# Kernel optimization log

Measured on AMD Instinct MI355X. Metric: run time of the kernel, lower is better.

Reference implementation:

```python
import jax, jax.numpy as jnp
import numpy as np

N_NODES = 100000
N_EDGES = 1600000
IN_CH = 128
OUT_CH = 64


def setup_inputs() -> dict:
    key = jax.random.key(0)
    k1, k2, k3, k4, k5 = jax.random.split(key, 5)
    x = jax.random.normal(k1, (N_NODES, IN_CH), dtype=jnp.float32)
    edge_index = jax.random.randint(k2, (2, N_EDGES), 0, N_NODES, dtype=jnp.int64)
    edge_weight = jax.random.uniform(k3, (N_EDGES,), dtype=jnp.float32)
    # GCNConv linear weight (glorot-ish scale) and bias
    W = jax.random.normal(k4, (IN_CH, OUT_CH), dtype=jnp.float32) / np.float32(np.sqrt(IN_CH))
    b = jax.random.normal(k5, (OUT_CH,), dtype=jnp.float32) * 0.01
    return {"x": x, "edge_index": edge_index, "edge_weight": edge_weight, "W": W, "b": b}


def reference(x, edge_index, edge_weight, W, b):
    # PyG GCNConv with add_self_loops=False, normalize=True, followed by Sigmoid.
    row = edge_index[0]  # source nodes [E]
    col = edge_index[1]  # target nodes [E]
    n = x.shape[0]

    # gcn_norm (no self loops): deg[j] = sum of edge_weight into j
    deg = jax.ops.segment_sum(edge_weight, col, num_segments=n)  # [N]
    deg_inv_sqrt = jnp.where(deg > 0, jax.lax.rsqrt(deg), jnp.float32(0))
    norm = deg_inv_sqrt[row] * edge_weight * deg_inv_sqrt[col]  # [E]

    # linear transform then gather-scale-scatter aggregation
    h = x @ W  # [N, OUT]
    msg = norm[:, None] * h[row]  # [E, OUT]
    out = jax.ops.segment_sum(msg, col, num_segments=n) + b  # [N, OUT]
    return jax.nn.sigmoid(out)
```

## Files before the change

### kernel.cpp

```cpp
#include <hip/hip_runtime.h>

#define IN_CH 128
#define OUT_CH 64
#define BN 64
#define CAP 1280
#define NPART 256

typedef __attribute__((ext_vector_type(8))) short short8;
typedef __attribute__((ext_vector_type(4))) float f32x4;

__device__ __forceinline__ unsigned short f2bf(float f) {
    unsigned u = __float_as_uint(f);
    unsigned r = (u + 0x7FFFu + ((u >> 16) & 1u)) >> 16;
    return (unsigned short)r;
}

__global__ __launch_bounds__(1024) void k_part2(const int* __restrict__ row,
                                                const int* __restrict__ col,
                                                const float* __restrict__ ew,
                                                int* __restrict__ cnt,
                                                uint2* __restrict__ sparse,
                                                int E, int per, int nbuck) {
    __shared__ uint2 srec[6272];
    __shared__ unsigned short sbin[6272];
    __shared__ int loff[1600];
    __shared__ int lcur[1600];
    __shared__ int gbase[1600];
    __shared__ int wpart[16];
    __shared__ int stot;

    int tid = threadIdx.x;
    int e0 = blockIdx.x * per;
    int e1 = min(E, e0 + per);
    int nloc = e1 - e0;

    for (int i = tid; i < nbuck; i += 1024) loff[i] = 0;
    __syncthreads();

    for (int e = e0 + tid; e < e1; e += 1024)
        atomicAdd(&loff[col[e] >> 6], 1);
    __syncthreads();

    int b0 = 2 * tid, b1 = 2 * tid + 1;
    int s0 = (b0 < nbuck) ? loff[b0] : 0;
    int s1 = (b1 < nbuck) ? loff[b1] : 0;
    int ts = s0 + s1;
    int lane = tid & 63, wv = tid >> 6;
    int v = ts;
#pragma unroll
    for (int d = 1; d < 64; d <<= 1) { int t = __shfl_up(v, d, 64); if (lane >= d) v += t; }
    if (lane == 63) wpart[wv] = v;
    __syncthreads();
    if (tid < 16) {
        int vv = wpart[tid];
#pragma unroll
        for (int d = 1; d < 16; d <<= 1) { int t = __shfl_up(vv, d, 16); if (tid >= d) vv += t; }
        wpart[tid] = vv;
        if (tid == 15) stot = vv;
    }
    __syncthreads();
    int excl = ((wv > 0) ? wpart[wv - 1] : 0) + (v - ts);
    if (b0 < nbuck) loff[b0] = excl;
    if (b1 < nbuck) loff[b1] = excl + s0;
    __syncthreads();

    int total = stot;
    for (int b = tid; b < nbuck; b += 1024) {
        int nxt = (b + 1 < nbuck) ? loff[b + 1] : total;
        int c = nxt - loff[b];
        gbase[b] = c ? atomicAdd(&cnt[b], c) : 0;
        lcur[b] = loff[b];
    }
    __syncthreads();

    for (int e = e0 + tid; e < e1; e += 1024) {
        int r = row[e];
        int c = col[e];
        float w = ew[e];
        int bin = c >> 6;
        int p = atomicAdd(&lcur[bin], 1);
        srec[p] = make_uint2((unsigned)r | ((unsigned)(c & 63) << 17),
                             __float_as_uint(w));
        sbin[p] = (unsigned short)bin;
    }
    __syncthreads();

    for (int i = tid; i < nloc; i += 1024) {
        int bin = sbin[i];
        int k = i - loff[bin];
        int gp = gbase[bin] + k;
        if (gp < CAP)
            sparse[(size_t)bin * CAP + gp] = srec[i];
    }
}

__global__ __launch_bounds__(256) void k_gemm3(const float* __restrict__ x,
                                               const float* __restrict__ W,
                                               const uint2* __restrict__ sparse,
                                               const int* __restrict__ cnt,
                                               float* __restrict__ dis,
                                               unsigned short* __restrict__ hb,
                                               int N) {
    __shared__ unsigned short Wl[64][136];
    __shared__ float degs[BN];

    int tid = threadIdx.x;
    int b = blockIdx.x;
    int row0 = b * BN;

    if (tid < BN) degs[tid] = 0.f;
    __syncthreads();

    for (int i = tid; i < 2048; i += 256) {
        int k = i >> 4;
        int n4 = (i & 15) << 2;
        float4 v = *(const float4*)(W + (size_t)k * OUT_CH + n4);
        Wl[n4 + 0][k] = f2bf(v.x);
        Wl[n4 + 1][k] = f2bf(v.y);
        Wl[n4 + 2][k] = f2bf(v.z);
        Wl[n4 + 3][k] = f2bf(v.w);
    }
    {
        int m = min(cnt[b], CAP);
        int sbase = b * CAP;
        for (int i = tid; i < m; i += 256) {
            uint2 r = sparse[sbase + i];
            atomicAdd(&degs[(r.x >> 17) & 63], __uint_as_float(r.y));
        }
    }
    __syncthreads();

    if (tid < BN) {
        float d = degs[tid];
        float dv = (d > 0.f) ? rsqrtf(d) : 0.f;
        int node = row0 + tid;
        if (node < N) dis[node] = dv;
        degs[tid] = dv;
    }

    int lane = tid & 63;
    int wv = tid >> 6;
    int r0l = 16 * wv;
    int cn = lane & 15;
    int rg = lane >> 4;

    f32x4 acc0 = {0.f, 0.f, 0.f, 0.f};
    f32x4 acc1 = {0.f, 0.f, 0.f, 0.f};
    f32x4 acc2 = {0.f, 0.f, 0.f, 0.f};
    f32x4 acc3 = {0.f, 0.f, 0.f, 0.f};

    int arow = row0 + r0l + cn;
#pragma unroll
    for (int ks = 0; ks < 4; ++ks) {
        int k0 = ks * 32 + rg * 8;
        short8 a = {};
        if (arow < N) {
            const float* xp = x + (size_t)arow * IN_CH + k0;
            float4 va = *(const float4*)(xp);
            float4 vb = *(const float4*)(xp + 4);
            a[0] = (short)f2bf(va.x); a[1] = (short)f2bf(va.y);
            a[2] = (short)f2bf(va.z); a[3] = (short)f2bf(va.w);
            a[4] = (short)f2bf(vb.x); a[5] = (short)f2bf(vb.y);
            a[6] = (short)f2bf(vb.z); a[7] = (short)f2bf(vb.w);
        }
        short8 b0 = *(const short8*)&Wl[ 0 + cn][k0];
        short8 b1 = *(const short8*)&Wl[16 + cn][k0];
        short8 b2 = *(const short8*)&Wl[32 + cn][k0];
        short8 b3 = *(const short8*)&Wl[48 + cn][k0];
        acc0 = __builtin_amdgcn_mfma_f32_16x16x32_bf16(a, b0, acc0, 0, 0, 0);
        acc1 = __builtin_amdgcn_mfma_f32_16x16x32_bf16(a, b1, acc1, 0, 0, 0);
        acc2 = __builtin_amdgcn_mfma_f32_16x16x32_bf16(a, b2, acc2, 0, 0, 0);
        acc3 = __builtin_amdgcn_mfma_f32_16x16x32_bf16(a, b3, acc3, 0, 0, 0);
    }
    __syncthreads();

#pragma unroll
    for (int r = 0; r < 4; ++r) {
        int row_l = r0l + rg * 4 + r;
        int grow = row0 + row_l;
        if (grow < N) {
            float sc = degs[row_l];
            unsigned short* hp = hb + (size_t)grow * OUT_CH + cn;
            hp[ 0] = f2bf(acc0[r] * sc);
            hp[16] = f2bf(acc1[r] * sc);
            hp[32] = f2bf(acc2[r] * sc);
            hp[48] = f2bf(acc3[r] * sc);
        }
    }
}

__global__ __launch_bounds__(256) void k_sort3(const uint2* __restrict__ sparse,
                                               const int* __restrict__ cnt,
                                               const float* __restrict__ dis,
                                               const unsigned short* __restrict__ hb,
                                               const float* __restrict__ bias,
                                               float* __restrict__ out,
                                               int N, int nbuck) {
    __shared__ uint2 recbuf[CAP];
    __shared__ uint2 recbuf2[CAP];
    __shared__ int hist[BN];
    __shared__ int cur[BN];
    __shared__ int starts[BN];

    int b = blockIdx.x;
    int tid = threadIdx.x;
    int sbase = b * CAP;
    int m = min(cnt[b], CAP);

    if (tid < BN) hist[tid] = 0;
    __syncthreads();

    for (int i = tid; i < m; i += 256) {
        uint2 r = sparse[sbase + i];
        recbuf[i] = r;
        atomicAdd(&hist[(r.x >> 17) & 63], 1);
    }
    __syncthreads();

    if (tid < 64) {
        int h = hist[tid];
        int v = h;
#pragma unroll
        for (int d = 1; d < 64; d <<= 1) {
            int t = __shfl_up(v, d, 64);
            if (tid >= d) v += t;
        }
        int excl = v - h;
        cur[tid] = excl;
        starts[tid] = excl;
    }
    __syncthreads();

    for (int i = tid; i < m; i += 256) {
        uint2 r = recbuf[i];
        int dl = (r.x >> 17) & 63;
        int p = atomicAdd(&cur[dl], 1);
        recbuf2[p] = make_uint2(r.x & 0x1FFFF, r.y);
    }
    __syncthreads();

    int hwl = tid >> 5;
    int lanep = tid & 31;
    unsigned co = 2u * (unsigned)lanep;
    for (int nl = hwl; nl < BN; nl += 8) {
        int node = b * BN + nl;
        if (node >= N) break;
        int e = starts[nl];
        int e1 = e + hist[nl];
        float accx = 0.f, accy = 0.f;
        for (; e + 3 < e1; e += 4) {
            uint2 p0 = recbuf2[e];
            uint2 p1 = recbuf2[e + 1];
            uint2 p2 = recbuf2[e + 2];
            uint2 p3 = recbuf2[e + 3];
            unsigned v0 = *(const unsigned*)(hb + (p0.x << 6) + co);
            unsigned v1 = *(const unsigned*)(hb + (p1.x << 6) + co);
            unsigned v2 = *(const unsigned*)(hb + (p2.x << 6) + co);
            unsigned v3 = *(const unsigned*)(hb + (p3.x << 6) + co);
            float w0 = __uint_as_float(p0.y), w1 = __uint_as_float(p1.y);
            float w2 = __uint_as_float(p2.y), w3 = __uint_as_float(p3.y);
            accx += w0 * __uint_as_float(v0 << 16);
            accy += w0 * __uint_as_float(v0 & 0xFFFF0000u);
            accx += w1 * __uint_as_float(v1 << 16);
            accy += w1 * __uint_as_float(v1 & 0xFFFF0000u);
            accx += w2 * __uint_as_float(v2 << 16);
            accy += w2 * __uint_as_float(v2 & 0xFFFF0000u);
            accx += w3 * __uint_as_float(v3 << 16);
            accy += w3 * __uint_as_float(v3 & 0xFFFF0000u);
        }
        for (; e < e1; ++e) {
            uint2 p = recbuf2[e];
            unsigned v = *(const unsigned*)(hb + (p.x << 6) + co);
            float w = __uint_as_float(p.y);
            accx += w * __uint_as_float(v << 16);
            accy += w * __uint_as_float(v & 0xFFFF0000u);
        }
        float dd = dis[node];
        float2 bb = *(const float2*)(bias + co);
        float2 o;
        o.x = 1.f / (1.f + __expf(-(accx * dd + bb.x)));
        o.y = 1.f / (1.f + __expf(-(accy * dd + bb.y)));
        *(float2*)(out + ((size_t)node << 6) + co) = o;
    }
}

extern "C" void kernel_launch(void* const* d_in, const int* in_sizes, int n_in,
                              void* d_out, int out_size, void* d_ws, size_t ws_size,
                              hipStream_t stream) {
    const float* x   = (const float*)d_in[0];
    const int*   ei  = (const int*)d_in[1];
    const float* ew  = (const float*)d_in[2];
    const float* W   = (const float*)d_in[3];
    const float* b   = (const float*)d_in[4];
    float* out = (float*)d_out;

    const int N = in_sizes[0] / IN_CH;
    const int E = in_sizes[1] / 2;
    const int* row = ei;
    const int* col = ei + E;

    const int nbuck = (N + BN - 1) / BN;
    const int per   = (E + NPART - 1) / NPART;

    char* p = (char*)d_ws;
    int*   cnt     = (int*)p;    p += (size_t)nbuck * 4;
    float* dis     = (float*)p;  p += (size_t)N * 4;
    uint2* sparse  = (uint2*)p;  p += (size_t)nbuck * CAP * 8;
    unsigned short* hb = (unsigned short*)p;

    hipMemsetAsync(cnt, 0, (size_t)nbuck * 4, stream);

    k_part2<<<NPART, 1024, 0, stream>>>(row, col, ew, cnt, sparse, E, per, nbuck);
    k_gemm3<<<nbuck, 256, 0, stream>>>(x, W, sparse, cnt, dis, hb, N);
    k_sort3<<<nbuck, 256, 0, stream>>>(sparse, cnt, dis, hb, b, out, N, nbuck);
}
```

Before: 192.1 us.

## Fuse partition, GEMM and aggregation into one cooperative persistent kernel

Replaces the three separate kernel launches with one cooperative kernel of 256 blocks of 1024 threads, separated by grid-wide syncs. The kernel first partitions edges by destination bucket, then computes degrees and the bf16 GEMM for four buckets per block at a time, then aggregates one bucket per block iteration. The aim is to remove launch and inter-kernel drain overhead. In exchange, each CU holds only one large block, so latency hiding in the gather-heavy aggregation drops, and grid syncs add their own cost.

```diff
diff --git a/kernel.cpp b/kernel.cpp
--- a/kernel.cpp
+++ b/kernel.cpp
@@ -1,10 +1,14 @@
 #include <hip/hip_runtime.h>
+#include <hip/hip_cooperative_groups.h>
+
+namespace cg = cooperative_groups;
 
 #define IN_CH 128
 #define OUT_CH 64
 #define BN 64
 #define CAP 1280
 #define NPART 256
+#define NBUCK_MAX 1600
 
 typedef __attribute__((ext_vector_type(8))) short short8;
 typedef __attribute__((ext_vector_type(4))) float f32x4;
@@ -15,272 +19,296 @@
     return (unsigned short)r;
 }
 
-__global__ __launch_bounds__(1024) void k_part2(const int* __restrict__ row,
-                                                const int* __restrict__ col,
-                                                const float* __restrict__ ew,
-                                                int* __restrict__ cnt,
-                                                uint2* __restrict__ sparse,
-                                                int E, int per, int nbuck) {
-    __shared__ uint2 srec[6272];
-    __shared__ unsigned short sbin[6272];
-    __shared__ int loff[1600];
-    __shared__ int lcur[1600];
-    __shared__ int gbase[1600];
-    __shared__ int wpart[16];
-    __shared__ int stot;
-
+struct PartSM {
+    uint2 srec[6272];
+    unsigned short sbin[6272];
+    int loff[NBUCK_MAX];
+    int lcur[NBUCK_MAX];
+    int gbase[NBUCK_MAX];
+    int wpart[16];
+    int stot;
+};
+struct GemmSM {
+    unsigned short Wl[64][136];
+    float degs[4][BN];
+};
+struct AggSM {
+    uint2 recbuf[CAP];
+    uint2 recbuf2[CAP];
+    int hist[BN];
+    int cur[BN];
+    int starts[BN];
+};
+union MegaSM { PartSM p; GemmSM g; AggSM a; };
+
+__global__ __launch_bounds__(1024, 4) void k_mega(const int* __restrict__ row,
+                                                  const int* __restrict__ col,
+                                                  const float* __restrict__ ew,
+                                                  const float* __restrict__ x,
+                                                  const float* __restrict__ W,
+                                                  const float* __restrict__ bias,
+                                                  int* __restrict__ cnt,
+                                                  float* __restrict__ dis,
+                                                  uint2* __restrict__ sparse,
+                                                  unsigned short* __restrict__ hb,
+                                                  float* __restrict__ out,
+                                                  int E, int per, int nbuck, int N) {
+    __shared__ MegaSM sm;
+    cg::grid_group grid = cg::this_grid();
     int tid = threadIdx.x;
-    int e0 = blockIdx.x * per;
-    int e1 = min(E, e0 + per);
-    int nloc = e1 - e0;
-
-    for (int i = tid; i < nbuck; i += 1024) loff[i] = 0;
-    __syncthreads();
-
-    for (int e = e0 + tid; e < e1; e += 1024)
-        atomicAdd(&loff[col[e] >> 6], 1);
-    __syncthreads();
-
-    int b0 = 2 * tid, b1 = 2 * tid + 1;
-    int s0 = (b0 < nbuck) ? loff[b0] : 0;
-    int s1 = (b1 < nbuck) ? loff[b1] : 0;
-    int ts = s0 + s1;
-    int lane = tid & 63, wv = tid >> 6;
-    int v = ts;
-#pragma unroll
-    for (int d = 1; d < 64; d <<= 1) { int t = __shfl_up(v, d, 64); if (lane >= d) v += t; }
-    if (lane == 63) wpart[wv] = v;
-    __syncthreads();
-    if (tid < 16) {
-        int vv = wpart[tid];
-#pragma unroll
-        for (int d = 1; d < 16; d <<= 1) { int t = __shfl_up(vv, d, 16); if (tid >= d) vv += t; }
-        wpart[tid] = vv;
-        if (tid == 15) stot = vv;
+    int bid = blockIdx.x;
+
+    {
+        int e0 = bid * per;
+        int e1 = min(E, e0 + per);
+        int nloc = e1 - e0;
+
+        for (int i = tid; i < nbuck; i += 1024) sm.p.loff[i] = 0;
+        __syncthreads();
+        for (int e = e0 + tid; e < e1; e += 1024)
+            atomicAdd(&sm.p.loff[col[e] >> 6], 1);
+        __syncthreads();
+
+        int b0 = 2 * tid, b1 = 2 * tid + 1;
+        int s0 = (b0 < nbuck) ? sm.p.loff[b0] : 0;
+        int s1 = (b1 < nbuck) ? sm.p.loff[b1] : 0;
+        int ts = s0 + s1;
+        int lane = tid & 63, wv = tid >> 6;
+        int v = ts;
+#pragma unroll
+        for (int d = 1; d < 64; d <<= 1) { int t = __shfl_up(v, d, 64); if (lane >= d) v += t; }
+        if (lane == 63) sm.p.wpart[wv] = v;
+        __syncthreads();
+        if (tid < 16) {
+            int vv = sm.p.wpart[tid];
+#pragma unroll
+            for (int d = 1; d < 16; d <<= 1) { int t = __shfl_up(vv, d, 16); if (tid >= d) vv += t; }
+            sm.p.wpart[tid] = vv;
+            if (tid == 15) sm.p.stot = vv;
+        }
+        __syncthreads();
+        int excl = ((wv > 0) ? sm.p.wpart[wv - 1] : 0) + (v - ts);
+        if (b0 < nbuck) sm.p.loff[b0] = excl;
+        if (b1 < nbuck) sm.p.loff[b1] = excl + s0;
+        __syncthreads();
+
+        int total = sm.p.stot;
+        for (int b = tid; b < nbuck; b += 1024) {
+            int nxt = (b + 1 < nbuck) ? sm.p.loff[b + 1] : total;
+            int c = nxt - sm.p.loff[b];
+            sm.p.gbase[b] = c ? atomicAdd(&cnt[b], c) : 0;
+            sm.p.lcur[b] = sm.p.loff[b];
+        }
+        __syncthreads();
+
+        for (int e = e0 + tid; e < e1; e += 1024) {
+            int r = row[e];
+            int c = col[e];
+            float w = ew[e];
+            int bin = c >> 6;
+            int p = atomicAdd(&sm.p.lcur[bin], 1);
+            sm.p.srec[p] = make_uint2((unsigned)r | ((unsigned)(c & 63) << 17),
+                                      __float_as_uint(w));
+            sm.p.sbin[p] = (unsigned short)bin;
+        }
+        __syncthreads();
+
+        for (int i = tid; i < nloc; i += 1024) {
+            int bin = sm.p.sbin[i];
+            int k = i - sm.p.loff[bin];
+            int gp = sm.p.gbase[bin] + k;
+            if (gp < CAP)
+                sparse[(size_t)bin * CAP + gp] = sm.p.srec[i];
+        }
     }
-    __syncthreads();
-    int excl = ((wv > 0) ? wpart[wv - 1] : 0) + (v - ts);
-    if (b0 < nbuck) loff[b0] = excl;
-    if (b1 < nbuck) loff[b1] = excl + s0;
-    __syncthreads();
-
-    int total = stot;
-    for (int b = tid; b < nbuck; b += 1024) {
-        int nxt = (b + 1 < nbuck) ? loff[b + 1] : total;
-        int c = nxt - loff[b];
-        gbase[b] = c ? atomicAdd(&cnt[b], c) : 0;
-        lcur[b] = loff[b];
+    __threadfence();
+    grid.sync();
+
+    {
+        for (int i = tid; i < 2048; i += 1024) {
+            int k = i >> 4;
+            int n4 = (i & 15) << 2;
+            float4 v = *(const float4*)(W + (size_t)k * OUT_CH + n4);
+            sm.g.Wl[n4 + 0][k] = f2bf(v.x);
+            sm.g.Wl[n4 + 1][k] = f2bf(v.y);
+            sm.g.Wl[n4 + 2][k] = f2bf(v.z);
+            sm.g.Wl[n4 + 3][k] = f2bf(v.w);
+        }
+        int tid_s = tid & 255;
+        int slot = tid >> 8;
+
+        for (int j = 0; j < 2; ++j) {
+            int b = bid + 256 * (4 * j + slot);
+            bool valid = b < nbuck;
+            int row0 = b * BN;
+
+            if (tid_s < BN) sm.g.degs[slot][tid_s] = 0.f;
+            __syncthreads();
+
+            if (valid) {
+                int m = min(cnt[b], CAP);
+                int sbase = b * CAP;
+                for (int i = tid_s; i < m; i += 256) {
+                    uint2 r = sparse[sbase + i];
+                    atomicAdd(&sm.g.degs[slot][(r.x >> 17) & 63], __uint_as_float(r.y));
+                }
+            }
+            __syncthreads();
+
+            if (valid && tid_s < BN) {
+                float d = sm.g.degs[slot][tid_s];
+                float dv = (d > 0.f) ? rsqrtf(d) : 0.f;
+                int node = row0 + tid_s;
+                if (node < N) dis[node] = dv;
+                sm.g.degs[slot][tid_s] = dv;
+            }
+
+            int lane = tid_s & 63;
+            int wvv = tid_s >> 6;
+            int r0l = 16 * wvv;
+            int cn = lane & 15;
+            int rg = lane >> 4;
+
+            f32x4 acc0 = {0.f, 0.f, 0.f, 0.f};
+            f32x4 acc1 = {0.f, 0.f, 0.f, 0.f};
+            f32x4 acc2 = {0.f, 0.f, 0.f, 0.f};
+            f32x4 acc3 = {0.f, 0.f, 0.f, 0.f};
+
+            if (valid) {
+                int arow = row0 + r0l + cn;
+#pragma unroll
+                for (int ks = 0; ks < 4; ++ks) {
+                    int k0 = ks * 32 + rg * 8;
+                    short8 a = {};
+                    if (arow < N) {
+                        const float* xp = x + (size_t)arow * IN_CH + k0;
+                        float4 va = *(const float4*)(xp);
+                        float4 vb = *(const float4*)(xp + 4);
+                        a[0] = (short)f2bf(va.x); a[1] = (short)f2bf(va.y);
+                        a[2] = (short)f2bf(va.z); a[3] = (short)f2bf(va.w);
+                        a[4] = (short)f2bf(vb.x); a[5] = (short)f2bf(vb.y);
+                        a[6] = (short)f2bf(vb.z); a[7] = (short)f2bf(vb.w);
+                    }
+                    short8 b0v = *(const short8*)&sm.g.Wl[ 0 + cn][k0];
+                    short8 b1v = *(const short8*)&sm.g.Wl[16 + cn][k0];
+                    short8 b2v = *(const short8*)&sm.g.Wl[32 + cn][k0];
+                    short8 b3v = *(const short8*)&sm.g.Wl[48 + cn][k0];
+                    acc0 = __builtin_amdgcn_mfma_f32_16x16x32_bf16(a, b0v, acc0, 0, 0, 0);
+                    acc1 = __builtin_amdgcn_mfma_f32_16x16x32_bf16(a, b1v, acc1, 0, 0, 0);
+                    acc2 = __builtin_amdgcn_mfma_f32_16x16x32_bf16(a, b2v, acc2, 0, 0, 0);
+                    acc3 = __builtin_amdgcn_mfma_f32_16x16x32_bf16(a, b3v, acc3, 0, 0, 0);
+                }
+            }
+            __syncthreads();
+
+            if (valid) {
+#pragma unroll
+                for (int r = 0; r < 4; ++r) {
+                    int row_l = r0l + rg * 4 + r;
+                    int grow = row0 + row_l;
+                    if (grow < N) {
+                        float sc = sm.g.degs[slot][row_l];
+                        unsigned short* hp = hb + (size_t)grow * OUT_CH + cn;
+                        hp[ 0] = f2bf(acc0[r] * sc);
+                        hp[16] = f2bf(acc1[r] * sc);
+                        hp[32] = f2bf(acc2[r] * sc);
+                        hp[48] = f2bf(acc3[r] * sc);
+                    }
+                }
+            }
+            __syncthreads();
+        }
     }
-    __syncthreads();
-
-    for (int e = e0 + tid; e < e1; e += 1024) {
-        int r = row[e];
-        int c = col[e];
-        float w = ew[e];
-        int bin = c >> 6;
-        int p = atomicAdd(&lcur[bin], 1);
-        srec[p] = make_uint2((unsigned)r | ((unsigned)(c & 63) << 17),
-                             __float_as_uint(w));
-        sbin[p] = (unsigned short)bin;
-    }
-    __syncthreads();
-
-    for (int i = tid; i < nloc; i += 1024) {
-        int bin = sbin[i];
-        int k = i - loff[bin];
-        int gp = gbase[bin] + k;
-        if (gp < CAP)
-            sparse[(size_t)bin * CAP + gp] = srec[i];
-    }
-}
-
-__global__ __launch_bounds__(256) void k_gemm3(const float* __restrict__ x,
-                                               const float* __restrict__ W,
-                                               const uint2* __restrict__ sparse,
-                                               const int* __restrict__ cnt,
-                                               float* __restrict__ dis,
-                                               unsigned short* __restrict__ hb,
-                                               int N) {
-    __shared__ unsigned short Wl[64][136];
-    __shared__ float degs[BN];
-
-    int tid = threadIdx.x;
-    int b = blockIdx.x;
-    int row0 = b * BN;
-
-    if (tid < BN) degs[tid] = 0.f;
-    __syncthreads();
-
-    for (int i = tid; i < 2048; i += 256) {
-        int k = i >> 4;
-        int n4 = (i & 15) << 2;
-        float4 v = *(const float4*)(W + (size_t)k * OUT_CH + n4);
-        Wl[n4 + 0][k] = f2bf(v.x);
-        Wl[n4 + 1][k] = f2bf(v.y);
-        Wl[n4 + 2][k] = f2bf(v.z);
-        Wl[n4 + 3][k] = f2bf(v.w);
-    }
+    __threadfence();
+    grid.sync();
+
     {
-        int m = min(cnt[b], CAP);
-        int sbase = b * CAP;
-        for (int i = tid; i < m; i += 256) {
-            uint2 r = sparse[sbase + i];
-            atomicAdd(&degs[(r.x >> 17) & 63], __uint_as_float(r.y));
-        }
-    }
-    __syncthreads();
-
-    if (tid < BN) {
-        float d = degs[tid];
-        float dv = (d > 0.f) ? rsqrtf(d) : 0.f;
-        int node = row0 + tid;
-        if (node < N) dis[node] = dv;
-        degs[tid] = dv;
-    }
-
-    int lane = tid & 63;
-    int wv = tid >> 6;
-    int r0l = 16 * wv;
-    int cn = lane & 15;
-    int rg = lane >> 4;
-
-    f32x4 acc0 = {0.f, 0.f, 0.f, 0.f};
-    f32x4 acc1 = {0.f, 0.f, 0.f, 0.f};
-    f32x4 acc2 = {0.f, 0.f, 0.f, 0.f};
-    f32x4 acc3 = {0.f, 0.f, 0.f, 0.f};
-
-    int arow = row0 + r0l + cn;
-#pragma unroll
-    for (int ks = 0; ks < 4; ++ks) {
-        int k0 = ks * 32 + rg * 8;
-        short8 a = {};
-        if (arow < N) {
-            const float* xp = x + (size_t)arow * IN_CH + k0;
-            float4 va = *(const float4*)(xp);
-            float4 vb = *(const float4*)(xp + 4);
-            a[0] = (short)f2bf(va.x); a[1] = (short)f2bf(va.y);
-            a[2] = (short)f2bf(va.z); a[3] = (short)f2bf(va.w);
-            a[4] = (short)f2bf(vb.x); a[5] = (short)f2bf(vb.y);
-            a[6] = (short)f2bf(vb.z); a[7] = (short)f2bf(vb.w);
-        }
-        short8 b0 = *(const short8*)&Wl[ 0 + cn][k0];
-        short8 b1 = *(const short8*)&Wl[16 + cn][k0];
-        short8 b2 = *(const short8*)&Wl[32 + cn][k0];
-        short8 b3 = *(const short8*)&Wl[48 + cn][k0];
-        acc0 = __builtin_amdgcn_mfma_f32_16x16x32_bf16(a, b0, acc0, 0, 0, 0);
-        acc1 = __builtin_amdgcn_mfma_f32_16x16x32_bf16(a, b1, acc1, 0, 0, 0);
-        acc2 = __builtin_amdgcn_mfma_f32_16x16x32_bf16(a, b2, acc2, 0, 0, 0);
-        acc3 = __builtin_amdgcn_mfma_f32_16x16x32_bf16(a, b3, acc3, 0, 0, 0);
-    }
-    __syncthreads();
-
-#pragma unroll
-    for (int r = 0; r < 4; ++r) {
-        int row_l = r0l + rg * 4 + r;
-        int grow = row0 + row_l;
-        if (grow < N) {
-            float sc = degs[row_l];
-            unsigned short* hp = hb + (size_t)grow * OUT_CH + cn;
-            hp[ 0] = f2bf(acc0[r] * sc);
-            hp[16] = f2bf(acc1[r] * sc);
-            hp[32] = f2bf(acc2[r] * sc);
-            hp[48] = f2bf(acc3[r] * sc);
-        }
-    }
-}
-
-__global__ __launch_bounds__(256) void k_sort3(const uint2* __restrict__ sparse,
-                                               const int* __restrict__ cnt,
-                                               const float* __restrict__ dis,
-                                               const unsigned short* __restrict__ hb,
-                                               const float* __restrict__ bias,
-                                               float* __restrict__ out,
-                                               int N, int nbuck) {
-    __shared__ uint2 recbuf[CAP];
-    __shared__ uint2 recbuf2[CAP];
-    __shared__ int hist[BN];
-    __shared__ int cur[BN];
-    __shared__ int starts[BN];
-
-    int b = blockIdx.x;
-    int tid = threadIdx.x;
-    int sbase = b * CAP;
-    int m = min(cnt[b], CAP);
-
-    if (tid < BN) hist[tid] = 0;
-    __syncthreads();
-
-    for (int i = tid; i < m; i += 256) {
-        uint2 r = sparse[sbase + i];
-        recbuf[i] = r;
-        atomicAdd(&hist[(r.x >> 17) & 63], 1);
-    }
-    __syncthreads();
-
-    if (tid < 64) {
-        int h = hist[tid];
-        int v = h;
-#pragma unroll
-        for (int d = 1; d < 64; d <<= 1) {
-            int t = __shfl_up(v, d, 64);
-            if (tid >= d) v += t;
-        }
-        int excl = v - h;
-        cur[tid] = excl;
-        starts[tid] = excl;
-    }
-    __syncthreads();
-
-    for (int i = tid; i < m; i += 256) {
-        uint2 r = recbuf[i];
-        int dl = (r.x >> 17) & 63;
-        int p = atomicAdd(&cur[dl], 1);
-        recbuf2[p] = make_uint2(r.x & 0x1FFFF, r.y);
-    }
-    __syncthreads();
-
-    int hwl = tid >> 5;
-    int lanep = tid & 31;
-    unsigned co = 2u * (unsigned)lanep;
-    for (int nl = hwl; nl < BN; nl += 8) {
-        int node = b * BN + nl;
-        if (node >= N) break;
-        int e = starts[nl];
-        int e1 = e + hist[nl];
-        float accx = 0.f, accy = 0.f;
-        for (; e + 3 < e1; e += 4) {
-            uint2 p0 = recbuf2[e];
-            uint2 p1 = recbuf2[e + 1];
-            uint2 p2 = recbuf2[e + 2];
-            uint2 p3 = recbuf2[e + 3];
-            unsigned v0 = *(const unsigned*)(hb + (p0.x << 6) + co);
-            unsigned v1 = *(const unsigned*)(hb + (p1.x << 6) + co);
-            unsigned v2 = *(const unsigned*)(hb + (p2.x << 6) + co);
-            unsigned v3 = *(const unsigned*)(hb + (p3.x << 6) + co);
-            float w0 = __uint_as_float(p0.y), w1 = __uint_as_float(p1.y);
-            float w2 = __uint_as_float(p2.y), w3 = __uint_as_float(p3.y);
-            accx += w0 * __uint_as_float(v0 << 16);
-            accy += w0 * __uint_as_float(v0 & 0xFFFF0000u);
-            accx += w1 * __uint_as_float(v1 << 16);
-            accy += w1 * __uint_as_float(v1 & 0xFFFF0000u);
-            accx += w2 * __uint_as_float(v2 << 16);
-            accy += w2 * __uint_as_float(v2 & 0xFFFF0000u);
-            accx += w3 * __uint_as_float(v3 << 16);
-            accy += w3 * __uint_as_float(v3 & 0xFFFF0000u);
-        }
-        for (; e < e1; ++e) {
-            uint2 p = recbuf2[e];
-            unsigned v = *(const unsigned*)(hb + (p.x << 6) + co);
-            float w = __uint_as_float(p.y);
-            accx += w * __uint_as_float(v << 16);
-            accy += w * __uint_as_float(v & 0xFFFF0000u);
-        }
-        float dd = dis[node];
-        float2 bb = *(const float2*)(bias + co);
-        float2 o;
-        o.x = 1.f / (1.f + __expf(-(accx * dd + bb.x)));
-        o.y = 1.f / (1.f + __expf(-(accy * dd + bb.y)));
-        *(float2*)(out + ((size_t)node << 6) + co) = o;
+        int lanep = tid & 31;
+        int hwl = tid >> 5;
+        unsigned co = 2u * (unsigned)lanep;
+
+        for (int j = 0; j < 7; ++j) {
+            int b = bid + 256 * j;
+            bool valid = b < nbuck;
+            int m = 0, sbase = 0;
+            if (valid) { m = min(cnt[b], CAP); sbase = b * CAP; }
+
+            if (tid < BN) sm.a.hist[tid] = 0;
+            __syncthreads();
+
+            for (int i = tid; i < m; i += 1024) {
+                uint2 r = sparse[sbase + i];
+                sm.a.recbuf[i] = r;
+                atomicAdd(&sm.a.hist[(r.x >> 17) & 63], 1);
+            }
+            __syncthreads();
+
+            if (tid < 64) {
+                int h = sm.a.hist[tid];
+                int v = h;
+#pragma unroll
+                for (int d = 1; d < 64; d <<= 1) {
+                    int t = __shfl_up(v, d, 64);
+                    if (tid >= d) v += t;
+                }
+                int excl = v - h;
+                sm.a.cur[tid] = excl;
+                sm.a.starts[tid] = excl;
+            }
+            __syncthreads();
+
+            for (int i = tid; i < m; i += 1024) {
+                uint2 r = sm.a.recbuf[i];
+                int dl = (r.x >> 17) & 63;
+                int p = atomicAdd(&sm.a.cur[dl], 1);
+                sm.a.recbuf2[p] = make_uint2(r.x & 0x1FFFF, r.y);
+            }
+            __syncthreads();
+
+            if (valid) {
+                for (int nl = hwl; nl < BN; nl += 32) {
+                    int node = b * BN + nl;
+                    if (node >= N) break;
+                    int e = sm.a.starts[nl];
+                    int e1 = e + sm.a.hist[nl];
+                    float accx = 0.f, accy = 0.f;
+                    for (; e + 3 < e1; e += 4) {
+                        uint2 p0 = sm.a.recbuf2[e];
+                        uint2 p1 = sm.a.recbuf2[e + 1];
+                        uint2 p2 = sm.a.recbuf2[e + 2];
+                        uint2 p3 = sm.a.recbuf2[e + 3];
+                        unsigned v0 = *(const unsigned*)(hb + (p0.x << 6) + co);
+                        unsigned v1 = *(const unsigned*)(hb + (p1.x << 6) + co);
+                        unsigned v2 = *(const unsigned*)(hb + (p2.x << 6) + co);
+                        unsigned v3 = *(const unsigned*)(hb + (p3.x << 6) + co);
+                        float w0 = __uint_as_float(p0.y), w1 = __uint_as_float(p1.y);
+                        float w2 = __uint_as_float(p2.y), w3 = __uint_as_float(p3.y);
+                        accx += w0 * __uint_as_float(v0 << 16);
+                        accy += w0 * __uint_as_float(v0 & 0xFFFF0000u);
+                        accx += w1 * __uint_as_float(v1 << 16);
+                        accy += w1 * __uint_as_float(v1 & 0xFFFF0000u);
+                        accx += w2 * __uint_as_float(v2 << 16);
+                        accy += w2 * __uint_as_float(v2 & 0xFFFF0000u);
+                        accx += w3 * __uint_as_float(v3 << 16);
+                        accy += w3 * __uint_as_float(v3 & 0xFFFF0000u);
+                    }
+                    for (; e < e1; ++e) {
+                        uint2 p = sm.a.recbuf2[e];
+                        unsigned vv = *(const unsigned*)(hb + (p.x << 6) + co);
+                        float w = __uint_as_float(p.y);
+                        accx += w * __uint_as_float(vv << 16);
+                        accy += w * __uint_as_float(vv & 0xFFFF0000u);
+                    }
+                    float dd = dis[node];
+                    float2 bb = *(const float2*)(bias + co);
+                    float2 o;
+                    o.x = 1.f / (1.f + __expf(-(accx * dd + bb.x)));
+                    o.y = 1.f / (1.f + __expf(-(accy * dd + bb.y)));
+                    *(float2*)(out + ((size_t)node << 6) + co) = o;
+                }
+            }
+            __syncthreads();
+        }
     }
 }
 
@@ -294,13 +322,13 @@
     const float* b   = (const float*)d_in[4];
     float* out = (float*)d_out;
 
-    const int N = in_sizes[0] / IN_CH;
-    const int E = in_sizes[1] / 2;
+    int N = in_sizes[0] / IN_CH;
+    int E = in_sizes[1] / 2;
     const int* row = ei;
     const int* col = ei + E;
 
-    const int nbuck = (N + BN - 1) / BN;
-    const int per   = (E + NPART - 1) / NPART;
+    int nbuck = (N + BN - 1) / BN;
+    int per   = (E + NPART - 1) / NPART;
 
     char* p = (char*)d_ws;
     int*   cnt     = (int*)p;    p += (size_t)nbuck * 4;
@@ -310,7 +338,9 @@
 
     hipMemsetAsync(cnt, 0, (size_t)nbuck * 4, stream);
 
-    k_part2<<<NPART, 1024, 0, stream>>>(row, col, ew, cnt, sparse, E, per, nbuck);
-    k_gemm3<<<nbuck, 256, 0, stream>>>(x, W, sparse, cnt, dis, hb, N);
-    k_sort3<<<nbuck, 256, 0, stream>>>(sparse, cnt, dis, hb, b, out, N, nbuck);
+    void* args[] = {(void*)&row, (void*)&col, (void*)&ew, (void*)&x, (void*)&W,
+                    (void*)&b, (void*)&cnt, (void*)&dis, (void*)&sparse,
+                    (void*)&hb, (void*)&out,
+                    (void*)&E, (void*)&per, (void*)&nbuck, (void*)&N};
+    hipLaunchCooperativeKernel((void*)k_mega, dim3(NPART), dim3(1024), args, 0, stream);
 }
```

Measured after the change: 491.9 us. 156% more time.
